# Kernel optimization log

Hardware: AMD Instinct MI355X
Metric: run time of the kernel (lower is better)

## Reference

```python
import jax, jax.numpy as jnp
import numpy as np

B, N, D = 4, 4096, 256
H = 4
HD = D // H
FF = max(2 * D, 16)
EPS = 1e-5


def layer_norm(x, w, b):
    mu = jnp.mean(x, axis=-1, keepdims=True)
    var = jnp.mean(jnp.square(x - mu), axis=-1, keepdims=True)
    return (x - mu) * jax.lax.rsqrt(var + EPS) * w + b


def setup_inputs() -> dict:
    key = jax.random.key(0)
    ks = jax.random.split(key, 12)
    s = 1.0 / np.sqrt(D)
    sf = 1.0 / np.sqrt(FF)
    return {
        "tokens": jax.random.normal(ks[0], (B, N, D), jnp.float32),
        "importance": jax.random.normal(ks[1], (B, N), jnp.float32),
        "norm1_w": jnp.ones((D,), jnp.float32),
        "norm1_b": jnp.zeros((D,), jnp.float32),
        "Wq": jax.random.uniform(ks[2], (D, D), jnp.float32, -s, s),
        "bq": jnp.zeros((D,), jnp.float32),
        "Wk": jax.random.uniform(ks[3], (D, D), jnp.float32, -s, s),
        "bk": jnp.zeros((D,), jnp.float32),
        "Wv": jax.random.uniform(ks[4], (D, D), jnp.float32, -s, s),
        "bv": jnp.zeros((D,), jnp.float32),
        "Wo": jax.random.uniform(ks[5], (D, D), jnp.float32, -s, s),
        "bo": jnp.zeros((D,), jnp.float32),
        "norm2_w": jnp.ones((D,), jnp.float32),
        "norm2_b": jnp.zeros((D,), jnp.float32),
        "W1": jax.random.uniform(ks[6], (D, FF), jnp.float32, -s, s),
        "b1": jnp.zeros((FF,), jnp.float32),
        "W2": jax.random.uniform(ks[7], (FF, D), jnp.float32, -sf, sf),
        "b2": jnp.zeros((D,), jnp.float32),
    }


def reference(tokens, importance, norm1_w, norm1_b, Wq, bq, Wk, bk, Wv, bv,
              Wo, bo, norm2_w, norm2_b, W1, b1, W2, b2):
    # pre-norm MHA with additive importance bias
    x = layer_norm(tokens, norm1_w, norm1_b)
    q = (x @ Wq + bq).reshape(B, N, H, HD).transpose(0, 2, 1, 3)  # [B,H,N,HD]
    k = (x @ Wk + bk).reshape(B, N, H, HD).transpose(0, 2, 1, 3)
    v = (x @ Wv + bv).reshape(B, N, H, HD).transpose(0, 2, 1, 3)
    scores = jnp.einsum("bhnd,bhmd->bhnm", q, k) / np.sqrt(HD)
    scores = scores + importance[:, None, None, :]  # bias over key dim
    attn = jax.nn.softmax(scores, axis=-1)
    ctx = jnp.einsum("bhnm,bhmd->bhnd", attn, v)
    ctx = ctx.transpose(0, 2, 1, 3).reshape(B, N, D)
    x = tokens + (ctx @ Wo + bo)
    # GELU FFN (exact erf gelu, matching torch default)
    y = layer_norm(x, norm2_w, norm2_b)
    y = jax.nn.gelu(y @ W1 + b1, approximate=False) @ W2 + b2
    return x + y
```

## Files before the change

kernel.cpp:

```cpp
#include <hip/hip_runtime.h>

#define Bb 4
#define Nn 4096
#define Dd 256
#define Hh 4
#define HDd 64
#define FFf 512
#define MT 16384

typedef __attribute__((ext_vector_type(8))) short short8;
typedef __attribute__((ext_vector_type(4))) float f32x4;
typedef __attribute__((ext_vector_type(16))) float f32x16;
typedef unsigned short u16;
typedef unsigned int u32;
typedef __attribute__((ext_vector_type(4))) u32 u32x4;

typedef __attribute__((address_space(1))) const void glb_src;
typedef __attribute__((address_space(3))) void lds_dst;

__device__ __forceinline__ void gload_lds16(const void* g, void* l) {
    __builtin_amdgcn_global_load_lds((glb_src*)g, (lds_dst*)l, 16, 0, 0);
}

__device__ __forceinline__ u16 f2bf(float f) {
    union { float f; u32 i; } v; v.f = f;
    u32 r = v.i + 0x7FFFu + ((v.i >> 16) & 1u);
    return (u16)(r >> 16);
}

__device__ __forceinline__ short8 ld8(const u16* p) {
    return *(const short8*)p;
}

__device__ __forceinline__ void pl32swap(u32& a, u32& b) {
    asm("v_permlane32_swap_b32 %0, %1" : "+v"(a), "+v"(b));
}
__device__ __forceinline__ float xhalf_max(float x) {
    u32 a = __float_as_uint(x), b = a;
    pl32swap(a, b);
    return fmaxf(__uint_as_float(a), __uint_as_float(b));
}
__device__ __forceinline__ u32 cvtpk(float lo, float hi) {
    u32 r;
    asm("v_cvt_pk_bf16_f32 %0, %1, %2" : "=v"(r) : "v"(lo), "v"(hi));
    return r;
}
__device__ __forceinline__ float fexp2(float x) {
    float r;
    asm("v_exp_f32 %0, %1" : "=v"(r) : "v"(x));
    return r;
}
__device__ __forceinline__ float max3f(float a, float b, float c) {
    float r;
    asm("v_max3_f32 %0, %1, %2, %3" : "=v"(r) : "v"(a), "v"(b), "v"(c));
    return r;
}

#define QSCALE 0.18033610062f
#define LOG2E  1.44269504089f

__global__ __launch_bounds__(256) void prep_kernel(
        const float* __restrict__ Wq, const float* __restrict__ Wk,
        const float* __restrict__ Wv, const float* __restrict__ Wo,
        const float* __restrict__ W1, const float* __restrict__ W2,
        const float* __restrict__ imp,
        u16* __restrict__ WqkvT, u16* __restrict__ WoT,
        u16* __restrict__ W1T, u16* __restrict__ W2T,
        u32* __restrict__ impPk) {
    int e = blockIdx.x * 256 + threadIdx.x;
    if (e < 196608) {
        int c = e >> 8, k = e & 255;
        int mat = c >> 8;
        int cc = c & 255;
        const float* W = (mat == 0) ? Wq : ((mat == 1) ? Wk : Wv);
        WqkvT[(size_t)c * 256 + k] = f2bf(W[k * 256 + cc]);
    } else if (e < 262144) {
        int i = e - 196608; int n = i >> 8, k = i & 255;
        WoT[n * 256 + k] = f2bf(Wo[k * 256 + n]);
    } else if (e < 393216) {
        int i = e - 262144; int n = i >> 8, k = i & 255;
        W1T[n * 256 + k] = f2bf(W1[k * 512 + n]);
    } else if (e < 524288) {
        int i = e - 393216; int n = i >> 9, k = i & 511;
        W2T[n * 512 + k] = f2bf(W2[k * 256 + n]);
    } else {
        int i = e - 524288;
        float ivs = imp[i] * LOG2E;
        u16 ih = f2bf(ivs);
        float rem = ivs - __uint_as_float(((u32)ih) << 16);
        u16 il = f2bf(rem);
        impPk[i] = ((u32)il << 16) | ih;
    }
}

__global__ __launch_bounds__(256) void ln_kernel(const float* __restrict__ x,
        const float* __restrict__ w, const float* __restrict__ bia,
        u16* __restrict__ out) {
    int lane = threadIdx.x & 63;
    int row = blockIdx.x * 4 + (threadIdx.x >> 6);
    const float* xr = x + (size_t)row * Dd;
    float4 v = *(const float4*)(xr + lane * 4);
    float s = v.x + v.y + v.z + v.w;
    float s2 = v.x * v.x + v.y * v.y + v.z * v.z + v.w * v.w;
    #pragma unroll
    for (int off = 1; off < 64; off <<= 1) {
        s  += __shfl_xor(s, off);
        s2 += __shfl_xor(s2, off);
    }
    float mu = s * (1.0f / Dd);
    float var = s2 * (1.0f / Dd) - mu * mu;
    float rstd = rsqrtf(var + 1e-5f);
    float4 wv = *(const float4*)(w + lane * 4);
    float4 bv = *(const float4*)(bia + lane * 4);
    ushort4 ov;
    ov.x = f2bf((v.x - mu) * rstd * wv.x + bv.x);
    ov.y = f2bf((v.y - mu) * rstd * wv.y + bv.y);
    ov.z = f2bf((v.z - mu) * rstd * wv.z + bv.z);
    ov.w = f2bf((v.w - mu) * rstd * wv.w + bv.w);
    *(ushort4*)(out + (size_t)row * Dd + lane * 4) = ov;
}

template<int MODE, int KD, int BM>
__global__ __launch_bounds__(256) void gemm_bt(
        const u16* __restrict__ A, const u16* __restrict__ BT,
        const float* __restrict__ bias0, const float* __restrict__ bias1,
        const float* __restrict__ bias2,
        const float* __restrict__ resid, float* __restrict__ outf,
        u16* __restrict__ o0, u16* __restrict__ o1, u16* __restrict__ o2) {
    constexpr int AM = BM / 32;
    __shared__ u16 Asl[BM * 32];
    __shared__ u16 Bsl[128 * 32];
    int lane = threadIdx.x & 63;
    int wv = threadIdx.x >> 6;
    int wm = wv >> 1, wn = wv & 1;
    int m0 = blockIdx.y * BM, n0 = blockIdx.x * 128;
    f32x4 zz; zz[0] = 0.f; zz[1] = 0.f; zz[2] = 0.f; zz[3] = 0.f;
    f32x4 acc[AM][4];
    #pragma unroll
    for (int i = 0; i < AM; ++i)
        #pragma unroll
        for (int j = 0; j < 4; ++j) acc[i][j] = zz;

    for (int kt = 0; kt < KD; kt += 32) {
        __syncthreads();
        #pragma unroll
        for (int i = 0; i < BM / 64; ++i) {
            int chunk = threadIdx.x + i * 256;
            int row = chunk >> 2, c16 = chunk & 3;
            int srcc = (c16 ^ (row & 3)) * 8;
            gload_lds16(A + (size_t)(m0 + row) * KD + kt + srcc,
                        (char*)Asl + wv * 1024 + i * 4096);
        }
        #pragma unroll
        for (int i = 0; i < 2; ++i) {
            int chunk = threadIdx.x + i * 256;
            int row = chunk >> 2, c16 = chunk & 3;
            int srcc = (c16 ^ (row & 3)) * 8;
            gload_lds16(BT + (size_t)(n0 + row) * KD + kt + srcc,
                        (char*)Bsl + wv * 1024 + i * 4096);
        }
        __syncthreads();
        short8 af[AM], bfr[4];
        #pragma unroll
        for (int t = 0; t < AM; ++t) {
            int arow = wm * (BM / 2) + t * 16 + (lane & 15);
            af[t] = ld8(Asl + arow * 32 + (((lane >> 4) * 8) ^ ((arow & 3) * 8)));
        }
        #pragma unroll
        for (int t = 0; t < 4; ++t) {
            int brow = wn * 64 + t * 16 + (lane & 15);
            bfr[t] = ld8(Bsl + brow * 32 + (((lane >> 4) * 8) ^ ((brow & 3) * 8)));
        }
        #pragma unroll
        for (int mt = 0; mt < AM; ++mt)
            #pragma unroll
            for (int nt = 0; nt < 4; ++nt)
                acc[mt][nt] = __builtin_amdgcn_mfma_f32_16x16x32_bf16(af[mt], bfr[nt], acc[mt][nt], 0, 0, 0);
    }

    #pragma unroll
    for (int mt = 0; mt < AM; ++mt) {
        #pragma unroll
        for (int nt = 0; nt < 4; ++nt) {
            #pragma unroll
            for (int r = 0; r < 4; ++r) {
                int row = m0 + wm * (BM / 2) + mt * 16 + (lane >> 4) * 4 + r;
                int col = n0 + wn * 64 + nt * 16 + (lane & 15);
                float v = acc[mt][nt][r];
                if (MODE == 0) {
                    int mat = col >> 8;
                    int cc = col & 255;
                    int hh = cc >> 6, dd = cc & 63;
                    int bbi = row >> 12, nni = row & 4095;
                    int bh = bbi * Hh + hh;
                    if (mat == 0)      o0[((size_t)bh * Nn + nni) * HDd + dd] = f2bf((v + bias0[cc]) * QSCALE);
                    else if (mat == 1) o1[((size_t)bh * Nn + nni) * HDd + dd] = f2bf(v + bias1[cc]);
                    else               o2[((size_t)bh * HDd + dd) * Nn + nni] = f2bf(v + bias2[cc]);
                } else if (MODE == 2) {
                    float xg = v + bias0[col];
                    float g = 0.5f * xg * (1.0f + erff(xg * 0.70710678118654752f));
                    o0[(size_t)row * FFf + col] = f2bf(g);
                } else {
                    outf[(size_t)row * Dd + col] = resid[(size_t)row * Dd + col] + v + bias0[col];
                }
            }
        }
    }
}

__global__ __launch_bounds__(256) void oproj_ln_kernel(
        const u16* __restrict__ A, const u16* __restrict__ BT,
        const float* __restrict__ bias, const float* __restrict__ resid,
        const float* __restrict__ lnw, const float* __restrict__ lnb,
        float* __restrict__ x2, u16* __restrict__ yln) {
    __shared__ u16 Asl[32 * 32];
    __shared__ u16 Bsl[256 * 32];
    __shared__ float xlds[32][256];
    int lane = threadIdx.x & 63;
    int wv = threadIdx.x >> 6;
    int m0 = blockIdx.x * 32;
    f32x4 zz; zz[0] = 0.f; zz[1] = 0.f; zz[2] = 0.f; zz[3] = 0.f;
    f32x4 acc[2][4];
    #pragma unroll
    for (int i = 0; i < 2; ++i)
        #pragma unroll
        for (int j = 0; j < 4; ++j) acc[i][j] = zz;

    for (int kt = 0; kt < Dd; kt += 32) {
        __syncthreads();
        if (wv < 2) {
            int t = threadIdx.x;
            int row = t >> 2, c16 = t & 3;
            int srcc = (c16 ^ (row & 3)) * 8;
            gload_lds16(A + (size_t)(m0 + row) * Dd + kt + srcc,
                        (char*)Asl + wv * 1024);
        }
        #pragma unroll
        for (int i = 0; i < 4; ++i) {
            int chunk = threadIdx.x + i * 256;
            int row = chunk >> 2, c16 = chunk & 3;
            int srcc = (c16 ^ (row & 3)) * 8;
            gload_lds16(BT + (size_t)row * Dd + kt + srcc,
                        (char*)Bsl + wv * 1024 + i * 4096);
        }
        __syncthreads();
        short8 af[2], bfr[4];
        #pragma unroll
        for (int t = 0; t < 2; ++t) {
            int arow = t * 16 + (lane & 15);
            af[t] = ld8(Asl + arow * 32 + (((lane >> 4) * 8) ^ ((arow & 3) * 8)));
        }
        #pragma unroll
        for (int t = 0; t < 4; ++t) {
            int brow = wv * 64 + t * 16 + (lane & 15);
            bfr[t] = ld8(Bsl + brow * 32 + (((lane >> 4) * 8) ^ ((brow & 3) * 8)));
        }
        #pragma unroll
        for (int mt = 0; mt < 2; ++mt)
            #pragma unroll
            for (int nt = 0; nt < 4; ++nt)
                acc[mt][nt] = __builtin_amdgcn_mfma_f32_16x16x32_bf16(af[mt], bfr[nt], acc[mt][nt], 0, 0, 0);
    }

    #pragma unroll
    for (int mt = 0; mt < 2; ++mt) {
        #pragma unroll
        for (int nt = 0; nt < 4; ++nt) {
            #pragma unroll
            for (int r = 0; r < 4; ++r) {
                int row = mt * 16 + (lane >> 4) * 4 + r;
                int col = wv * 64 + nt * 16 + (lane & 15);
                float v = resid[(size_t)(m0 + row) * Dd + col] + acc[mt][nt][r] + bias[col];
                x2[(size_t)(m0 + row) * Dd + col] = v;
                xlds[row][col] = v;
            }
        }
    }
    __syncthreads();

    int rw = threadIdx.x >> 3;
    int cg = (threadIdx.x & 7) * 32;
    float s = 0.f, s2 = 0.f;
    #pragma unroll
    for (int j = 0; j < 32; ++j) {
        float v = xlds[rw][cg + j];
        s += v; s2 += v * v;
    }
    #pragma unroll
    for (int off = 1; off < 8; off <<= 1) {
        s  += __shfl_xor(s, off);
        s2 += __shfl_xor(s2, off);
    }
    float mu = s * (1.0f / Dd);
    float var = s2 * (1.0f / Dd) - mu * mu;
    float rstd = rsqrtf(var + 1e-5f);
    u16* op = yln + (size_t)(m0 + rw) * Dd + cg;
    #pragma unroll
    for (int j = 0; j < 32; j += 8) {
        float v0 = (xlds[rw][cg + j + 0] - mu) * rstd * lnw[cg + j + 0] + lnb[cg + j + 0];
        float v1 = (xlds[rw][cg + j + 1] - mu) * rstd * lnw[cg + j + 1] + lnb[cg + j + 1];
        float v2 = (xlds[rw][cg + j + 2] - mu) * rstd * lnw[cg + j + 2] + lnb[cg + j + 2];
        float v3 = (xlds[rw][cg + j + 3] - mu) * rstd * lnw[cg + j + 3] + lnb[cg + j + 3];
        float v4 = (xlds[rw][cg + j + 4] - mu) * rstd * lnw[cg + j + 4] + lnb[cg + j + 4];
        float v5 = (xlds[rw][cg + j + 5] - mu) * rstd * lnw[cg + j + 5] + lnb[cg + j + 5];
        float v6 = (xlds[rw][cg + j + 6] - mu) * rstd * lnw[cg + j + 6] + lnb[cg + j + 6];
        float v7 = (xlds[rw][cg + j + 7] - mu) * rstd * lnw[cg + j + 7] + lnb[cg + j + 7];
        uint4 pk;
        pk.x = cvtpk(v0, v1); pk.y = cvtpk(v2, v3);
        pk.z = cvtpk(v4, v5); pk.w = cvtpk(v6, v7);
        *(uint4*)(op + j) = pk;
    }
}

__global__ __launch_bounds__(256, 2) void attn_kernel(
        const u16* __restrict__ Qb, const u16* __restrict__ Kb,
        const u16* __restrict__ VTb, const u32* __restrict__ impPk,
        u16* __restrict__ pc, float* __restrict__ pm, float* __restrict__ pl) {
    __shared__ u16 Klds[2][64 * 64];
    __shared__ u16 Vlds[2][64 * 64];
    int lane = threadIdx.x & 63;
    int wv = threadIdx.x >> 6;
    int kvh = blockIdx.x >> 8;
    int bh = (blockIdx.x >> 4) & 15;
    int qt = blockIdx.x & 15;
    int bbi = bh >> 2;
    int qrow0 = qt * 256 + wv * 64;
    int q = lane & 31;
    int hf = lane >> 5;
    int key0 = kvh * 2048;
    int pg = kvh * 16 + bh;

    short8 qfA[4], qfB[4];
    #pragma unroll
    for (int ks = 0; ks < 4; ++ks) {
        qfA[ks] = ld8(Qb + ((size_t)bh * Nn + qrow0 + q) * HDd + ks * 16 + hf * 8);
        qfB[ks] = ld8(Qb + ((size_t)bh * Nn + qrow0 + 32 + q) * HDd + ks * 16 + hf * 8);
    }

    short8 onef = (short8)0;
    if (hf == 0) { onef[0] = (short)0x3F80; onef[1] = (short)0x3F80; }
    short8 aoneLo = (short8)0, aoneHi = (short8)0;
    if ((lane & 31) < 16) {
        #pragma unroll
        for (int j = 0; j < 8; ++j) aoneLo[j] = (short)0x3F80;
    } else {
        #pragma unroll
        for (int j = 0; j < 8; ++j) aoneHi[j] = (short)0x3F80;
    }

    int sr = lane >> 3;
    int sc = lane & 7;
    int swz = (sc ^ sr) * 8;
    const u16* kp = Kb + ((size_t)bh * Nn + key0 + wv * 16 + sr) * HDd + swz;
    const u16* vp = VTb + ((size_t)bh * HDd + wv * 16 + sr) * Nn + key0 + swz;
    size_t ib = (size_t)bbi * Nn;

    gload_lds16(kp,           (char*)Klds[0] + wv * 2048);
    gload_lds16(kp + 8 * HDd, (char*)Klds[0] + wv * 2048 + 1024);
    gload_lds16(vp,           (char*)Vlds[0] + wv * 2048);
    gload_lds16(vp + 8 * Nn,  (char*)Vlds[0] + wv * 2048 + 1024);
    kp += 64 * HDd; vp += 64;
    u32 npk0 = impPk[ib + key0 + q], npk1 = impPk[ib + key0 + 32 + q];

    f32x16 ctxA[2], ctxB[2], lacc;
    #pragma unroll
    for (int r = 0; r < 16; ++r) {
        ctxA[0][r] = 0.f; ctxA[1][r] = 0.f;
        ctxB[0][r] = 0.f; ctxB[1][r] = 0.f;
        lacc[r] = 0.f;
    }
    float mA = -__builtin_inff(), mB = -__builtin_inff();

    int cur = 0;
    for (int t = 0; t < 32; ++t) {
        __syncthreads();
        u32 pk0 = npk0, pk1 = npk1;
        if (t < 31) {
            gload_lds16(kp,           (char*)Klds[cur ^ 1] + wv * 2048);
            gload_lds16(kp + 8 * HDd, (char*)Klds[cur ^ 1] + wv * 2048 + 1024);
            gload_lds16(vp,           (char*)Vlds[cur ^ 1] + wv * 2048);
            gload_lds16(vp + 8 * Nn,  (char*)Vlds[cur ^ 1] + wv * 2048 + 1024);
            kp += 64 * HDd; vp += 64;
            npk0 = impPk[ib + key0 + t * 64 + 64 + q];
            npk1 = impPk[ib + key0 + t * 64 + 96 + q];
        }
        const u16* Kc = Klds[cur];
        const u16* Vc = Vlds[cur];

        f32x16 sA0, sA1, sB0, sB1;
        #pragma unroll
        for (int r = 0; r < 16; ++r) { sA0[r] = 0.f; sA1[r] = 0.f; sB0[r] = 0.f; sB1[r] = 0.f; }
        __builtin_amdgcn_s_setprio(1);
        #pragma unroll
        for (int ks = 0; ks < 4; ++ks) {
            short8 kf0 = ld8(Kc + q * 64 + (((ks * 2 + hf) ^ (q & 7)) * 8));
            short8 kf1 = ld8(Kc + (32 + q) * 64 + (((ks * 2 + hf) ^ (q & 7)) * 8));
            sA0 = __builtin_amdgcn_mfma_f32_32x32x16_bf16(kf0, qfA[ks], sA0, 0, 0, 0);
            sA1 = __builtin_amdgcn_mfma_f32_32x32x16_bf16(kf1, qfA[ks], sA1, 0, 0, 0);
            sB0 = __builtin_amdgcn_mfma_f32_32x32x16_bf16(kf0, qfB[ks], sB0, 0, 0, 0);
            sB1 = __builtin_amdgcn_mfma_f32_32x32x16_bf16(kf1, qfB[ks], sB1, 0, 0, 0);
        }
        short8 af0 = (short8)0, af1 = (short8)0;
        if (hf == 0) {
            af0[0] = (short)(pk0 & 0xFFFFu); af0[1] = (short)(pk0 >> 16);
            af1[0] = (short)(pk1 & 0xFFFFu); af1[1] = (short)(pk1 >> 16);
        }
        sA0 = __builtin_amdgcn_mfma_f32_32x32x16_bf16(af0, onef, sA0, 0, 0, 0);
        sA1 = __builtin_amdgcn_mfma_f32_32x32x16_bf16(af1, onef, sA1, 0, 0, 0);
        sB0 = __builtin_amdgcn_mfma_f32_32x32x16_bf16(af0, onef, sB0, 0, 0, 0);
        sB1 = __builtin_amdgcn_mfma_f32_32x32x16_bf16(af1, onef, sB1, 0, 0, 0);
        __builtin_amdgcn_s_setprio(0);

        {
            float a0 = max3f(sA0[0], sA0[1], sA0[2]);
            float a1 = max3f(sA0[3], sA0[4], sA0[5]);
            float a2 = max3f(sA0[6], sA0[7], sA0[8]);
            float a3 = max3f(sA0[9], sA0[10], sA0[11]);
            float a4 = max3f(sA0[12], sA0[13], sA0[14]);
            float b0 = max3f(sA1[0], sA1[1], sA1[2]);
            float b1 = max3f(sA1[3], sA1[4], sA1[5]);
            float b2 = max3f(sA1[6], sA1[7], sA1[8]);
            float b3 = max3f(sA1[9], sA1[10], sA1[11]);
            float b4 = max3f(sA1[12], sA1[13], sA1[14]);
            float c0 = max3f(a0, a1, a2);
            float c1 = max3f(a3, a4, sA0[15]);
            float c2 = max3f(b0, b1, b2);
            float c3 = max3f(b3, b4, sA1[15]);
            float tm = xhalf_max(fmaxf(max3f(c0, c1, c2), c3));
            bool nore = __all(tm <= mA + 8.0f);
            if (!nore) {
                float nm = fmaxf(mA, tm);
                float al = fexp2(mA - nm);
                #pragma unroll
                for (int r = 0; r < 8; ++r) lacc[r] *= al;
                #pragma unroll
                for (int r = 0; r < 16; ++r) { ctxA[0][r] *= al; ctxA[1][r] *= al; }
                mA = nm;
            }
            #pragma unroll
            for (int r = 0; r < 16; ++r) { sA0[r] = fexp2(sA0[r] - mA); sA1[r] = fexp2(sA1[r] - mA); }
        }
        {
            float a0 = max3f(sB0[0], sB0[1], sB0[2]);
            float a1 = max3f(sB0[3], sB0[4], sB0[5]);
            float a2 = max3f(sB0[6], sB0[7], sB0[8]);
            float a3 = max3f(sB0[9], sB0[10], sB0[11]);
            float a4 = max3f(sB0[12], sB0[13], sB0[14]);
            float b0 = max3f(sB1[0], sB1[1], sB1[2]);
            float b1 = max3f(sB1[3], sB1[4], sB1[5]);
            float b2 = max3f(sB1[6], sB1[7], sB1[8]);
            float b3 = max3f(sB1[9], sB1[10], sB1[11]);
            float b4 = max3f(sB1[12], sB1[13], sB1[14]);
            float c0 = max3f(a0, a1, a2);
            float c1 = max3f(a3, a4, sB0[15]);
            float c2 = max3f(b0, b1, b2);
            float c3 = max3f(b3, b4, sB1[15]);
            float tm = xhalf_max(fmaxf(max3f(c0, c1, c2), c3));
            bool nore = __all(tm <= mB + 8.0f);
            if (!nore) {
                float nm = fmaxf(mB, tm);
                float al = fexp2(mB - nm);
                #pragma unroll
                for (int r = 8; r < 16; ++r) lacc[r] *= al;
                #pragma unroll
                for (int r = 0; r < 16; ++r) { ctxB[0][r] *= al; ctxB[1][r] *= al; }
                mB = nm;
            }
            #pragma unroll
            for (int r = 0; r < 16; ++r) { sB0[r] = fexp2(sB0[r] - mB); sB1[r] = fexp2(sB1[r] - mB); }
        }

        u32 wA0[8], wA1[8], wB0[8], wB1[8];
        #pragma unroll
        for (int j = 0; j < 8; ++j) {
            wA0[j] = cvtpk(sA0[2 * j], sA0[2 * j + 1]);
            wA1[j] = cvtpk(sA1[2 * j], sA1[2 * j + 1]);
            wB0[j] = cvtpk(sB0[2 * j], sB0[2 * j + 1]);
            wB1[j] = cvtpk(sB1[2 * j], sB1[2 * j + 1]);
        }
        pl32swap(wA0[0], wA0[2]); pl32swap(wA0[1], wA0[3]);
        pl32swap(wA0[4], wA0[6]); pl32swap(wA0[5], wA0[7]);
        pl32swap(wA1[0], wA1[2]); pl32swap(wA1[1], wA1[3]);
        pl32swap(wA1[4], wA1[6]); pl32swap(wA1[5], wA1[7]);
        pl32swap(wB0[0], wB0[2]); pl32swap(wB0[1], wB0[3]);
        pl32swap(wB0[4], wB0[6]); pl32swap(wB0[5], wB0[7]);
        pl32swap(wB1[0], wB1[2]); pl32swap(wB1[1], wB1[3]);
        pl32swap(wB1[4], wB1[6]); pl32swap(wB1[5], wB1[7]);
        short8 pfA[4], pfB[4];
        {
            u32x4 t0; t0[0] = wA0[0]; t0[1] = wA0[1]; t0[2] = wA0[2]; t0[3] = wA0[3];
            u32x4 t1; t1[0] = wA0[4]; t1[1] = wA0[5]; t1[2] = wA0[6]; t1[3] = wA0[7];
            u32x4 t2; t2[0] = wA1[0]; t2[1] = wA1[1]; t2[2] = wA1[2]; t2[3] = wA1[3];
            u32x4 t3; t3[0] = wA1[4]; t3[1] = wA1[5]; t3[2] = wA1[6]; t3[3] = wA1[7];
            pfA[0] = __builtin_bit_cast(short8, t0);
            pfA[1] = __builtin_bit_cast(short8, t1);
            pfA[2] = __builtin_bit_cast(short8, t2);
            pfA[3] = __builtin_bit_cast(short8, t3);
            u32x4 u0; u0[0] = wB0[0]; u0[1] = wB0[1]; u0[2] = wB0[2]; u0[3] = wB0[3];
            u32x4 u1; u1[0] = wB0[4]; u1[1] = wB0[5]; u1[2] = wB0[6]; u1[3] = wB0[7];
            u32x4 u2; u2[0] = wB1[0]; u2[1] = wB1[1]; u2[2] = wB1[2]; u2[3] = wB1[3];
            u32x4 u3; u3[0] = wB1[4]; u3[1] = wB1[5]; u3[2] = wB1[6]; u3[3] = wB1[7];
            pfB[0] = __builtin_bit_cast(short8, u0);
            pfB[1] = __builtin_bit_cast(short8, u1);
            pfB[2] = __builtin_bit_cast(short8, u2);
            pfB[3] = __builtin_bit_cast(short8, u3);
        }

        __builtin_amdgcn_s_setprio(1);
        #pragma unroll
        for (int j = 0; j < 4; ++j) {
            lacc = __builtin_amdgcn_mfma_f32_32x32x16_bf16(aoneLo, pfA[j], lacc, 0, 0, 0);
            lacc = __builtin_amdgcn_mfma_f32_32x32x16_bf16(aoneHi, pfB[j], lacc, 0, 0, 0);
        }
        #pragma unroll
        for (int dt = 0; dt < 2; ++dt) {
            int vrow = dt * 32 + q;
            const u16* vb = Vc + vrow * 64;
            int sw = vrow & 7;
            #pragma unroll
            for (int j = 0; j < 4; ++j) {
                short8 vf = ld8(vb + (((2 * j + hf) ^ sw) * 8));
                ctxA[dt] = __builtin_amdgcn_mfma_f32_32x32x16_bf16(vf, pfA[j], ctxA[dt], 0, 0, 0);
                ctxB[dt] = __builtin_amdgcn_mfma_f32_32x32x16_bf16(vf, pfB[j], ctxB[dt], 0, 0, 0);
            }
        }
        __builtin_amdgcn_s_setprio(0);
        cur ^= 1;
    }

    int qgA = qrow0 + q, qgB = qrow0 + 32 + q;
    if (hf == 0) {
        pm[(size_t)pg * Nn + qgA] = mA;
        pl[(size_t)pg * Nn + qgA] = lacc[0];
        pm[(size_t)pg * Nn + qgB] = mB;
        pl[(size_t)pg * Nn + qgB] = lacc[8];
    }
    #pragma unroll
    for (int dt = 0; dt < 2; ++dt) {
        #pragma unroll
        for (int r = 0; r < 16; ++r) {
            int d = dt * 32 + (r & 3) + 8 * (r >> 2) + 4 * hf;
            pc[((size_t)pg * 64 + d) * Nn + qgA] = f2bf(ctxA[dt][r]);
            pc[((size_t)pg * 64 + d) * Nn + qgB] = f2bf(ctxB[dt][r]);
        }
    }
}

__global__ __launch_bounds__(256) void merge_kernel(
        const u16* __restrict__ pc, const float* __restrict__ pm,
        const float* __restrict__ pl, u16* __restrict__ ctxOut) {
    __shared__ float trans[64][65];
    __shared__ float f0a[64], f1a[64];
    int bh = blockIdx.x >> 6;
    int q0 = (blockIdx.x & 63) * 64;
    int t = threadIdx.x;
    if (t < 64) {
        int qg = q0 + t;
        float m0 = pm[(size_t)bh * Nn + qg];
        float m1 = pm[(size_t)(16 + bh) * Nn + qg];
        float l0 = pl[(size_t)bh * Nn + qg];
        float l1 = pl[(size_t)(16 + bh) * Nn + qg];
        float M = fmaxf(m0, m1);
        float w0 = fexp2(m0 - M), w1 = fexp2(m1 - M);
        float inv = 1.0f / (l0 * w0 + l1 * w1);
        f0a[t] = w0 * inv; f1a[t] = w1 * inv;
    }
    __syncthreads();
    int wv = t >> 6, lane = t & 63;
    #pragma unroll
    for (int i = 0; i < 16; ++i) {
        int d = wv * 16 + i;
        float c0 = __uint_as_float((u32)pc[((size_t)bh * 64 + d) * Nn + q0 + lane] << 16);
        float c1 = __uint_as_float((u32)pc[((size_t)(16 + bh) * 64 + d) * Nn + q0 + lane] << 16);
        trans[lane][d] = c0 * f0a[lane] + c1 * f1a[lane];
    }
    __syncthreads();
    int q = t >> 2, dg = t & 3;
    int b = bh >> 2, h = bh & 3;
    const float* tr = &trans[q][dg * 16];
    uint4 pa, pb;
    pa.x = cvtpk(tr[0], tr[1]);  pa.y = cvtpk(tr[2], tr[3]);
    pa.z = cvtpk(tr[4], tr[5]);  pa.w = cvtpk(tr[6], tr[7]);
    pb.x = cvtpk(tr[8], tr[9]);  pb.y = cvtpk(tr[10], tr[11]);
    pb.z = cvtpk(tr[12], tr[13]); pb.w = cvtpk(tr[14], tr[15]);
    u16* op = ctxOut + ((size_t)b * Nn + q0 + q) * Dd + h * 64 + dg * 16;
    *(uint4*)op = pa;
    *(uint4*)(op + 8) = pb;
}

extern "C" void kernel_launch(void* const* d_in, const int* in_sizes, int n_in,
                              void* d_out, int out_size, void* d_ws, size_t ws_size,
                              hipStream_t stream) {
    (void)in_sizes; (void)n_in; (void)out_size; (void)ws_size;
    const float* tokens     = (const float*)d_in[0];
    const float* importance = (const float*)d_in[1];
    const float* n1w = (const float*)d_in[2];
    const float* n1b = (const float*)d_in[3];
    const float* Wq  = (const float*)d_in[4];
    const float* bq  = (const float*)d_in[5];
    const float* Wk  = (const float*)d_in[6];
    const float* bk  = (const float*)d_in[7];
    const float* Wv  = (const float*)d_in[8];
    const float* bv  = (const float*)d_in[9];
    const float* Wo  = (const float*)d_in[10];
    const float* bo  = (const float*)d_in[11];
    const float* n2w = (const float*)d_in[12];
    const float* n2b = (const float*)d_in[13];
    const float* W1  = (const float*)d_in[14];
    const float* b1  = (const float*)d_in[15];
    const float* W2  = (const float*)d_in[16];
    const float* b2  = (const float*)d_in[17];
    float* out = (float*)d_out;

    char* ws = (char*)d_ws;
    const size_t MB = (size_t)1 << 20;
    u16* xln   = (u16*)(ws);
    u16* qb    = (u16*)(ws + 8 * MB);
    u16* kb    = (u16*)(ws + 16 * MB);
    u16* vT    = (u16*)(ws + 24 * MB);
    u16* ctx   = (u16*)(ws + 32 * MB);
    u16* pc    = (u16*)(ws + 40 * MB);
    float* pm  = (float*)(ws + 56 * MB);
    float* pl  = (float*)(ws + 56 * MB + 524288);
    u16* WqkvT = (u16*)(ws + 57 * MB);
    u16* WoT   = (u16*)(ws + 57 * MB + 393216);
    u16* W1T   = (u16*)(ws + 57 * MB + 393216 + 131072);
    u16* W2T   = (u16*)(ws + 57 * MB + 393216 + 131072 + 262144);
    u32* impPk = (u32*)(ws + 57 * MB + 393216 + 131072 + 262144 + 262144);
    u16* yln   = xln;
    u16* hbuf  = qb;
    float* x2  = out;

    prep_kernel<<<2112, 256, 0, stream>>>(Wq, Wk, Wv, Wo, W1, W2, importance,
                                          WqkvT, WoT, W1T, W2T, impPk);
    ln_kernel<<<4096, 256, 0, stream>>>(tokens, n1w, n1b, xln);
    gemm_bt<0, 256, 128><<<dim3(6, 128), 256, 0, stream>>>(xln, WqkvT, bq, bk, bv,
                                                           nullptr, nullptr, qb, kb, vT);
    attn_kernel<<<512, 256, 0, stream>>>(qb, kb, vT, impPk, pc, pm, pl);
    merge_kernel<<<1024, 256, 0, stream>>>(pc, pm, pl, ctx);
    oproj_ln_kernel<<<512, 256, 0, stream>>>(ctx, WoT, bo, tokens, n2w, n2b, x2, yln);
    gemm_bt<2, 256, 64><<<dim3(4, 256), 256, 0, stream>>>(yln, W1T, b1, nullptr, nullptr,
                                                          nullptr, nullptr, hbuf, nullptr, nullptr);
    gemm_bt<3, 512, 64><<<dim3(2, 256), 256, 0, stream>>>(hbuf, W2T, b2, nullptr, nullptr,
                                                          x2, out, nullptr, nullptr, nullptr);
}
```

Measured before the change: 183.1 us.

## Split attention key range four ways and merge four partial softmax results

The attention kernel now splits the 4096 keys into four chunks of 1024 instead of two of 2048, doubling the grid to 1024 blocks and raising the launch-bounds occupancy hint to 4 blocks per SM. The merge kernel combines four partial (max, sum, context) sets instead of two, and the workspace layout moves to fit the larger partial-context buffer. The aim is to fill the 256 CUs of the MI355X better, since 512 blocks left many idle. The cost is twice the partial-output traffic and a heavier merge, plus register pressure from the tighter launch bound that may cause spills.

Result: slower. 630.4 us (+244.4%).

```diff
diff --git a/kernel.cpp b/kernel.cpp
--- a/kernel.cpp
+++ b/kernel.cpp
@@ -312,7 +312,7 @@
     }
 }
 
-__global__ __launch_bounds__(256, 2) void attn_kernel(
+__global__ __launch_bounds__(256, 4) void attn_kernel(
         const u16* __restrict__ Qb, const u16* __restrict__ Kb,
         const u16* __restrict__ VTb, const u32* __restrict__ impPk,
         u16* __restrict__ pc, float* __restrict__ pm, float* __restrict__ pl) {
@@ -320,15 +320,15 @@
     __shared__ u16 Vlds[2][64 * 64];
     int lane = threadIdx.x & 63;
     int wv = threadIdx.x >> 6;
-    int kvh = blockIdx.x >> 8;
+    int kvq = blockIdx.x >> 8;
     int bh = (blockIdx.x >> 4) & 15;
     int qt = blockIdx.x & 15;
     int bbi = bh >> 2;
     int qrow0 = qt * 256 + wv * 64;
     int q = lane & 31;
     int hf = lane >> 5;
-    int key0 = kvh * 2048;
-    int pg = kvh * 16 + bh;
+    int key0 = kvq * 1024;
+    int pg = kvq * 16 + bh;
 
     short8 qfA[4], qfB[4];
     #pragma unroll
@@ -372,10 +372,10 @@
     float mA = -__builtin_inff(), mB = -__builtin_inff();
 
     int cur = 0;
-    for (int t = 0; t < 32; ++t) {
+    for (int t = 0; t < 16; ++t) {
         __syncthreads();
         u32 pk0 = npk0, pk1 = npk1;
-        if (t < 31) {
+        if (t < 15) {
             gload_lds16(kp,           (char*)Klds[cur ^ 1] + wv * 2048);
             gload_lds16(kp + 8 * HDd, (char*)Klds[cur ^ 1] + wv * 2048 + 1024);
             gload_lds16(vp,           (char*)Vlds[cur ^ 1] + wv * 2048);
@@ -550,29 +550,39 @@
         const u16* __restrict__ pc, const float* __restrict__ pm,
         const float* __restrict__ pl, u16* __restrict__ ctxOut) {
     __shared__ float trans[64][65];
-    __shared__ float f0a[64], f1a[64];
+    __shared__ float fw[4][64];
     int bh = blockIdx.x >> 6;
     int q0 = (blockIdx.x & 63) * 64;
     int t = threadIdx.x;
     if (t < 64) {
         int qg = q0 + t;
-        float m0 = pm[(size_t)bh * Nn + qg];
+        float m0 = pm[(size_t)(bh) * Nn + qg];
         float m1 = pm[(size_t)(16 + bh) * Nn + qg];
-        float l0 = pl[(size_t)bh * Nn + qg];
-        float l1 = pl[(size_t)(16 + bh) * Nn + qg];
-        float M = fmaxf(m0, m1);
+        float m2 = pm[(size_t)(32 + bh) * Nn + qg];
+        float m3 = pm[(size_t)(48 + bh) * Nn + qg];
+        float M = fmaxf(fmaxf(m0, m1), fmaxf(m2, m3));
         float w0 = fexp2(m0 - M), w1 = fexp2(m1 - M);
-        float inv = 1.0f / (l0 * w0 + l1 * w1);
-        f0a[t] = w0 * inv; f1a[t] = w1 * inv;
+        float w2 = fexp2(m2 - M), w3 = fexp2(m3 - M);
+        float l = pl[(size_t)(bh) * Nn + qg] * w0
+                + pl[(size_t)(16 + bh) * Nn + qg] * w1
+                + pl[(size_t)(32 + bh) * Nn + qg] * w2
+                + pl[(size_t)(48 + bh) * Nn + qg] * w3;
+        float inv = 1.0f / l;
+        fw[0][t] = w0 * inv; fw[1][t] = w1 * inv;
+        fw[2][t] = w2 * inv; fw[3][t] = w3 * inv;
     }
     __syncthreads();
     int wv = t >> 6, lane = t & 63;
     #pragma unroll
     for (int i = 0; i < 16; ++i) {
         int d = wv * 16 + i;
-        float c0 = __uint_as_float((u32)pc[((size_t)bh * 64 + d) * Nn + q0 + lane] << 16);
-        float c1 = __uint_as_float((u32)pc[((size_t)(16 + bh) * 64 + d) * Nn + q0 + lane] << 16);
-        trans[lane][d] = c0 * f0a[lane] + c1 * f1a[lane];
+        float acc = 0.f;
+        #pragma unroll
+        for (int j = 0; j < 4; ++j) {
+            float c = __uint_as_float((u32)pc[((size_t)(j * 16 + bh) * 64 + d) * Nn + q0 + lane] << 16);
+            acc += c * fw[j][lane];
+        }
+        trans[lane][d] = acc;
     }
     __syncthreads();
     int q = t >> 2, dg = t & 3;
@@ -620,13 +630,13 @@
     u16* vT    = (u16*)(ws + 24 * MB);
     u16* ctx   = (u16*)(ws + 32 * MB);
     u16* pc    = (u16*)(ws + 40 * MB);
-    float* pm  = (float*)(ws + 56 * MB);
-    float* pl  = (float*)(ws + 56 * MB + 524288);
-    u16* WqkvT = (u16*)(ws + 57 * MB);
-    u16* WoT   = (u16*)(ws + 57 * MB + 393216);
-    u16* W1T   = (u16*)(ws + 57 * MB + 393216 + 131072);
-    u16* W2T   = (u16*)(ws + 57 * MB + 393216 + 131072 + 262144);
-    u32* impPk = (u32*)(ws + 57 * MB + 393216 + 131072 + 262144 + 262144);
+    float* pm  = (float*)(ws + 72 * MB);
+    float* pl  = (float*)(ws + 73 * MB);
+    u16* WqkvT = (u16*)(ws + 74 * MB);
+    u16* WoT   = (u16*)(ws + 74 * MB + 393216);
+    u16* W1T   = (u16*)(ws + 74 * MB + 393216 + 131072);
+    u16* W2T   = (u16*)(ws + 74 * MB + 393216 + 131072 + 262144);
+    u32* impPk = (u32*)(ws + 74 * MB + 393216 + 131072 + 262144 + 262144);
     u16* yln   = xln;
     u16* hbuf  = qb;
     float* x2  = out;
@@ -636,7 +646,7 @@
     ln_kernel<<<4096, 256, 0, stream>>>(tokens, n1w, n1b, xln);
     gemm_bt<0, 256, 128><<<dim3(6, 128), 256, 0, stream>>>(xln, WqkvT, bq, bk, bv,
                                                            nullptr, nullptr, qb, kb, vT);
-    attn_kernel<<<512, 256, 0, stream>>>(qb, kb, vT, impPk, pc, pm, pl);
+    attn_kernel<<<1024, 256, 0, stream>>>(qb, kb, vT, impPk, pc, pm, pl);
     merge_kernel<<<1024, 256, 0, stream>>>(pc, pm, pl, ctx);
     oproj_ln_kernel<<<512, 256, 0, stream>>>(ctx, WoT, bo, tokens, n2w, n2b, x2, yln);
     gemm_bt<2, 256, 64><<<dim3(4, 256), 256, 0, stream>>>(yln, W1T, b1, nullptr, nullptr,
```

## Fuse split-KV attention merge into output-projection LayerNorm kernel

Applied to the files above, without the earlier changes.

Removes the separate merge kernel and moves the combination of the two split-KV partial contexts (rescaling by max/sum statistics) into the prologue of the output-projection kernel. Each block now builds its full 32x256 bf16 A tile in LDS once from the partial context buffers, instead of loading it per k-step from a materialized ctx buffer. This saves a kernel launch and a full write and read of the ctx tensor. In exchange the prologue does strided, scalar-ish reads of the transposed partial buffers and more LDS traffic before the GEMM starts, which could reduce overlap.

Result: no change. 182.2 us (-0.5%).

```diff
diff --git a/kernel.cpp b/kernel.cpp
--- a/kernel.cpp
+++ b/kernel.cpp
@@ -209,16 +209,60 @@
 }
 
 __global__ __launch_bounds__(256) void oproj_ln_kernel(
-        const u16* __restrict__ A, const u16* __restrict__ BT,
+        const u16* __restrict__ pc, const float* __restrict__ pm,
+        const float* __restrict__ pl, const u16* __restrict__ BT,
         const float* __restrict__ bias, const float* __restrict__ resid,
         const float* __restrict__ lnw, const float* __restrict__ lnb,
         float* __restrict__ x2, u16* __restrict__ yln) {
-    __shared__ u16 Asl[32 * 32];
+    __shared__ u16 Asl[8][32 * 32];
     __shared__ u16 Bsl[256 * 32];
     __shared__ float xlds[32][256];
+    __shared__ float f0a[32][4], f1a[32][4];
     int lane = threadIdx.x & 63;
     int wv = threadIdx.x >> 6;
     int m0 = blockIdx.x * 32;
+    int b = m0 >> 12;
+    int n0 = m0 & 4095;
+
+    if (threadIdx.x < 128) {
+        int i = threadIdx.x >> 2, h = threadIdx.x & 3;
+        int bh = b * 4 + h;
+        int n = n0 + i;
+        float m0v = pm[(size_t)bh * Nn + n];
+        float m1v = pm[(size_t)(16 + bh) * Nn + n];
+        float l0 = pl[(size_t)bh * Nn + n];
+        float l1 = pl[(size_t)(16 + bh) * Nn + n];
+        float M = fmaxf(m0v, m1v);
+        float w0 = fexp2(m0v - M), w1 = fexp2(m1v - M);
+        float inv = 1.0f / (l0 * w0 + l1 * w1);
+        f0a[i][h] = w0 * inv;
+        f1a[i][h] = w1 * inv;
+    }
+    __syncthreads();
+
+    {
+        int c = threadIdx.x;
+        int h = c >> 6, d = c & 63;
+        int bh = b * 4 + h;
+        const u16* p0 = pc + ((size_t)bh * 64 + d) * Nn + n0;
+        const u16* p1 = pc + ((size_t)(16 + bh) * 64 + d) * Nn + n0;
+        int chunk = c >> 5, cc = c & 31;
+        u16* dst = &Asl[chunk][0];
+        #pragma unroll
+        for (int i0 = 0; i0 < 32; i0 += 8) {
+            short8 v0 = ld8(p0 + i0);
+            short8 v1 = ld8(p1 + i0);
+            #pragma unroll
+            for (int j = 0; j < 8; ++j) {
+                int i = i0 + j;
+                float c0 = __uint_as_float((u32)(unsigned short)v0[j] << 16);
+                float c1 = __uint_as_float((u32)(unsigned short)v1[j] << 16);
+                float v = c0 * f0a[i][h] + c1 * f1a[i][h];
+                dst[i * 32 + (((cc >> 3) ^ (i & 3)) * 8) + (cc & 7)] = f2bf(v);
+            }
+        }
+    }
+
     f32x4 zz; zz[0] = 0.f; zz[1] = 0.f; zz[2] = 0.f; zz[3] = 0.f;
     f32x4 acc[2][4];
     #pragma unroll
@@ -228,13 +272,6 @@
 
     for (int kt = 0; kt < Dd; kt += 32) {
         __syncthreads();
-        if (wv < 2) {
-            int t = threadIdx.x;
-            int row = t >> 2, c16 = t & 3;
-            int srcc = (c16 ^ (row & 3)) * 8;
-            gload_lds16(A + (size_t)(m0 + row) * Dd + kt + srcc,
-                        (char*)Asl + wv * 1024);
-        }
         #pragma unroll
         for (int i = 0; i < 4; ++i) {
             int chunk = threadIdx.x + i * 256;
@@ -245,10 +282,11 @@
         }
         __syncthreads();
         short8 af[2], bfr[4];
+        const u16* Ac = &Asl[kt >> 5][0];
         #pragma unroll
         for (int t = 0; t < 2; ++t) {
             int arow = t * 16 + (lane & 15);
-            af[t] = ld8(Asl + arow * 32 + (((lane >> 4) * 8) ^ ((arow & 3) * 8)));
+            af[t] = ld8(Ac + arow * 32 + (((lane >> 4) * 8) ^ ((arow & 3) * 8)));
         }
         #pragma unroll
         for (int t = 0; t < 4; ++t) {
@@ -546,48 +584,6 @@
     }
 }
 
-__global__ __launch_bounds__(256) void merge_kernel(
-        const u16* __restrict__ pc, const float* __restrict__ pm,
-        const float* __restrict__ pl, u16* __restrict__ ctxOut) {
-    __shared__ float trans[64][65];
-    __shared__ float f0a[64], f1a[64];
-    int bh = blockIdx.x >> 6;
-    int q0 = (blockIdx.x & 63) * 64;
-    int t = threadIdx.x;
-    if (t < 64) {
-        int qg = q0 + t;
-        float m0 = pm[(size_t)bh * Nn + qg];
-        float m1 = pm[(size_t)(16 + bh) * Nn + qg];
-        float l0 = pl[(size_t)bh * Nn + qg];
-        float l1 = pl[(size_t)(16 + bh) * Nn + qg];
-        float M = fmaxf(m0, m1);
-        float w0 = fexp2(m0 - M), w1 = fexp2(m1 - M);
-        float inv = 1.0f / (l0 * w0 + l1 * w1);
-        f0a[t] = w0 * inv; f1a[t] = w1 * inv;
-    }
-    __syncthreads();
-    int wv = t >> 6, lane = t & 63;
-    #pragma unroll
-    for (int i = 0; i < 16; ++i) {
-        int d = wv * 16 + i;
-        float c0 = __uint_as_float((u32)pc[((size_t)bh * 64 + d) * Nn + q0 + lane] << 16);
-        float c1 = __uint_as_float((u32)pc[((size_t)(16 + bh) * 64 + d) * Nn + q0 + lane] << 16);
-        trans[lane][d] = c0 * f0a[lane] + c1 * f1a[lane];
-    }
-    __syncthreads();
-    int q = t >> 2, dg = t & 3;
-    int b = bh >> 2, h = bh & 3;
-    const float* tr = &trans[q][dg * 16];
-    uint4 pa, pb;
-    pa.x = cvtpk(tr[0], tr[1]);  pa.y = cvtpk(tr[2], tr[3]);
-    pa.z = cvtpk(tr[4], tr[5]);  pa.w = cvtpk(tr[6], tr[7]);
-    pb.x = cvtpk(tr[8], tr[9]);  pb.y = cvtpk(tr[10], tr[11]);
-    pb.z = cvtpk(tr[12], tr[13]); pb.w = cvtpk(tr[14], tr[15]);
-    u16* op = ctxOut + ((size_t)b * Nn + q0 + q) * Dd + h * 64 + dg * 16;
-    *(uint4*)op = pa;
-    *(uint4*)(op + 8) = pb;
-}
-
 extern "C" void kernel_launch(void* const* d_in, const int* in_sizes, int n_in,
                               void* d_out, int out_size, void* d_ws, size_t ws_size,
                               hipStream_t stream) {
@@ -618,7 +614,6 @@
     u16* qb    = (u16*)(ws + 8 * MB);
     u16* kb    = (u16*)(ws + 16 * MB);
     u16* vT    = (u16*)(ws + 24 * MB);
-    u16* ctx   = (u16*)(ws + 32 * MB);
     u16* pc    = (u16*)(ws + 40 * MB);
     float* pm  = (float*)(ws + 56 * MB);
     float* pl  = (float*)(ws + 56 * MB + 524288);
@@ -637,8 +632,8 @@
     gemm_bt<0, 256, 128><<<dim3(6, 128), 256, 0, stream>>>(xln, WqkvT, bq, bk, bv,
                                                            nullptr, nullptr, qb, kb, vT);
     attn_kernel<<<512, 256, 0, stream>>>(qb, kb, vT, impPk, pc, pm, pl);
-    merge_kernel<<<1024, 256, 0, stream>>>(pc, pm, pl, ctx);
-    oproj_ln_kernel<<<512, 256, 0, stream>>>(ctx, WoT, bo, tokens, n2w, n2b, x2, yln);
+    oproj_ln_kernel<<<512, 256, 0, stream>>>(pc, pm, pl, WoT, bo, tokens,
+                                             n2w, n2b, x2, yln);
     gemm_bt<2, 256, 64><<<dim3(4, 256), 256, 0, stream>>>(yln, W1T, b1, nullptr, nullptr,
                                                           nullptr, nullptr, hbuf, nullptr, nullptr);
     gemm_bt<3, 512, 64><<<dim3(2, 256), 256, 0, stream>>>(hbuf, W2T, b2, nullptr, nullptr,
```
